# Kernel tuning notes

Hardware: AMD Instinct MI355X
Metric: run time of the kernel (lower is better)

The kernel has to match this reference:

```python
import jax, jax.numpy as jnp
import numpy as np

B, D, S, U, H = 2, 1024, 2048, 1024, 16
LN_EPS = 1e-5

def setup_inputs() -> dict:
    key = jax.random.key(0)
    ks = jax.random.split(key, 5)
    std = 0.02
    return {
        "inputs": jax.random.normal(ks[0], (B, D, S), jnp.float32),
        "Wq": jax.random.normal(ks[1], (D, U), jnp.float32) * std,
        "bq": jnp.zeros((U,), jnp.float32),
        "Wk": jax.random.normal(ks[2], (D, U), jnp.float32) * std,
        "bk": jnp.zeros((U,), jnp.float32),
        "Wv": jax.random.normal(ks[3], (D, U), jnp.float32) * std,
        "bv": jnp.zeros((U,), jnp.float32),
        "Wo": jax.random.normal(ks[4], (U, D), jnp.float32) * std,
        "bo": jnp.zeros((D,), jnp.float32),
        "gamma": jnp.ones((D,), jnp.float32),
        "beta": jnp.zeros((D,), jnp.float32),
        "num_heads": H,
    }

def reference(inputs, Wq, bq, Wk, bk, Wv, bv, Wo, bo, gamma, beta, num_heads):
    # inputs: (B, D, S) -> (B, S, D)
    x = jnp.transpose(inputs, (0, 2, 1))
    b, s, d = x.shape

    def proj(W, bias):
        y = jax.nn.relu(x @ W + bias)               # (b, s, U)
        y = y.reshape(b, s, num_heads, -1)
        return jnp.transpose(y, (0, 2, 1, 3))       # (b, h, s, hd)

    Q = proj(Wq, bq)
    K = proj(Wk, bk)
    V = proj(Wv, bv)
    hd = Q.shape[-1]
    scale = 1.0 / np.sqrt(hd).astype(np.float32)

    # Block-wise flash attention in the source is mathematically plain softmax attention
    # (per-block epsilon 1e-10 is negligible); scale applied to Q, no mask, no dropout.
    scores = jnp.einsum('bhid,bhjd->bhij', Q * scale, K)   # (b, h, s, s)
    P = jax.nn.softmax(scores, axis=-1)
    O = jnp.einsum('bhij,bhjd->bhid', P, V)                # (b, h, s, hd)

    O = jnp.transpose(O, (0, 2, 1, 3)).reshape(b, s, -1)   # (b, s, U)
    out = O @ Wo + bo + x                                  # residual add
    mean = jnp.mean(out, axis=-1, keepdims=True)
    var = jnp.var(out, axis=-1, keepdims=True)
    y = (out - mean) * jax.lax.rsqrt(var + LN_EPS) * gamma + beta
    return jnp.transpose(y, (0, 2, 1))                     # (B, D, S)
```

## Files before the change

### kernel.cpp

```cpp
#include <hip/hip_runtime.h>
#include <hip/hip_bf16.h>

typedef __bf16 bf16x8 __attribute__((ext_vector_type(8)));
typedef __bf16 bf16x4 __attribute__((ext_vector_type(4)));
typedef float  f32x4  __attribute__((ext_vector_type(4)));
typedef float  f32x16 __attribute__((ext_vector_type(16)));

#define MFMA16(a, b, c) __builtin_amdgcn_mfma_f32_16x16x32_bf16((a), (b), (c), 0, 0, 0)
#define MFMA32(a, b, c) __builtin_amdgcn_mfma_f32_32x32x16_bf16((a), (b), (c), 0, 0, 0)

namespace {
constexpr int Bb = 2, Dd = 1024, Ss = 2048, Uu = 1024, Hh = 16;
}

#if __has_builtin(__builtin_amdgcn_exp2f)
#define EXP2(x) __builtin_amdgcn_exp2f(x)
#else
#define EXP2(x) __expf((x) * 0.6931471805599453f)
#endif

__device__ __forceinline__ uint32_t pkbf(float a, float b) {
  union { __bf16 h[2]; uint32_t u; } z;
  z.h[0] = (__bf16)a; z.h[1] = (__bf16)b;
  return z.u;
}
#define PLSWAP(a, b) asm("v_permlane32_swap_b32 %0, %1" : "+v"(a), "+v"(b))

__device__ __forceinline__ void gl16(const void* g, void* l) {
  __builtin_amdgcn_global_load_lds((const __attribute__((address_space(1))) uint32_t*)g,
                                   (__attribute__((address_space(3))) uint32_t*)l, 16, 0, 0);
}

#define VMW(n) asm volatile("s_waitcnt vmcnt(" #n ")" ::: "memory")
#define BARRIER_PIN() do { __builtin_amdgcn_s_barrier(); \
  asm volatile("" ::: "memory"); __builtin_amdgcn_sched_barrier(0); } while (0)
#define LGKM0() asm volatile("s_waitcnt lgkmcnt(0)" ::: "memory")

__global__ __launch_bounds__(256) void k_xpose_x(const float* __restrict__ inp,
                                                 __bf16* __restrict__ xb, float* __restrict__ xt) {
  __shared__ __attribute__((aligned(16))) float xs[64][65];
  const int s0 = blockIdx.x * 64, d0 = blockIdx.y * 64, b = blockIdx.z;
  const int t = threadIdx.x;
  {
    const int i = t >> 2, c = (t & 3) * 16;
    const float* src = inp + ((size_t)(b * Dd + d0 + i)) * Ss + s0 + c;
#pragma unroll
    for (int q = 0; q < 4; ++q) {
      const float4 f = *(const float4*)(src + q * 4);
      xs[i][c + q * 4 + 0] = f.x; xs[i][c + q * 4 + 1] = f.y;
      xs[i][c + q * 4 + 2] = f.z; xs[i][c + q * 4 + 3] = f.w;
    }
  }
  __syncthreads();
  {
    const int sl = t >> 2, dc = (t & 3) * 16;
    float* dstf = xt + ((size_t)(b * Ss + s0 + sl)) * Dd + d0 + dc;
    bf16x8 va, vb;
#pragma unroll
    for (int q = 0; q < 4; ++q) {
      float4 f;
      f.x = xs[dc + q * 4 + 0][sl]; f.y = xs[dc + q * 4 + 1][sl];
      f.z = xs[dc + q * 4 + 2][sl]; f.w = xs[dc + q * 4 + 3][sl];
      *(float4*)(dstf + q * 4) = f;
    }
#pragma unroll
    for (int j = 0; j < 8; ++j) { va[j] = (__bf16)xs[dc + j][sl]; vb[j] = (__bf16)xs[dc + 8 + j][sl]; }
    __bf16* dst = xb + ((size_t)(b * Ss + s0 + sl)) * Dd + d0 + dc;
    *(bf16x8*)dst = va;
    *(bf16x8*)(dst + 8) = vb;
  }
}

__global__ __launch_bounds__(256) void k_xpose_w(const float* __restrict__ w0, const float* __restrict__ w1,
                                                 const float* __restrict__ w2, const float* __restrict__ w3,
                                                 __bf16* __restrict__ o0, __bf16* __restrict__ o1,
                                                 __bf16* __restrict__ o2, __bf16* __restrict__ o3) {
  __shared__ __attribute__((aligned(16))) __bf16 ts[64][72];
  const float* src_m; __bf16* dst_m;
  switch (blockIdx.z) {
    case 0: src_m = w0; dst_m = o0; break;
    case 1: src_m = w1; dst_m = o1; break;
    case 2: src_m = w2; dst_m = o2; break;
    default: src_m = w3; dst_m = o3; break;
  }
  const int n0 = blockIdx.x * 64, k0 = blockIdx.y * 64;
  const int t = threadIdx.x;
  {
    const int i = t >> 2, c = (t & 3) * 16;
    const float* src = src_m + (size_t)(k0 + i) * 1024 + n0 + c;
#pragma unroll
    for (int q = 0; q < 4; ++q) {
      const float4 f = *(const float4*)(src + q * 4);
      ts[i][c + q * 4 + 0] = (__bf16)f.x;
      ts[i][c + q * 4 + 1] = (__bf16)f.y;
      ts[i][c + q * 4 + 2] = (__bf16)f.z;
      ts[i][c + q * 4 + 3] = (__bf16)f.w;
    }
  }
  __syncthreads();
  {
    const int nl = t >> 2, kc = (t & 3) * 16;
    bf16x8 va, vb;
#pragma unroll
    for (int j = 0; j < 8; ++j) { va[j] = ts[kc + j][nl]; vb[j] = ts[kc + 8 + j][nl]; }
    __bf16* dst = dst_m + (size_t)(n0 + nl) * 1024 + k0 + kc;
    *(bf16x8*)dst = va;
    *(bf16x8*)(dst + 8) = vb;
  }
}

__global__ __launch_bounds__(512, 2) void k_gemm_qkv8(const __bf16* __restrict__ A,
    const __bf16* __restrict__ W0, const __bf16* __restrict__ W1, const __bf16* __restrict__ W2,
    const float* __restrict__ b0, const float* __restrict__ b1, const float* __restrict__ b2,
    __bf16* __restrict__ Qb, __bf16* __restrict__ Kb, __bf16* __restrict__ Vt) {
  __shared__ __attribute__((aligned(16))) __bf16 As[4][256][32];
  __shared__ __attribute__((aligned(16))) __bf16 Bs[4][256][32];
  const int t = threadIdx.x;
  const int w = t >> 6, l = t & 63, lg = l >> 4, lr = l & 15;
  const int wm = w >> 2, wn = w & 3;
  const int bid = blockIdx.x;
  const int logical = (bid & 7) * 24 + (bid >> 3);
  const int z = logical >> 6;
  const int rem = logical & 63;
  const int n0 = (rem & 3) * 256, m0 = (rem >> 2) * 256;
  const __bf16* Bt = z == 0 ? W0 : z == 1 ? W1 : W2;
  const float* bias = z == 0 ? b0 : z == 1 ? b1 : b2;

  const int srow = t >> 2, sc8 = t & 3, scol = sc8 * 8;
  const int so = ((sc8 + 4 - ((srow >> 1) & 3)) & 3) * 8;
  const __bf16* gaB = A  + ((size_t)(m0 + srow)) * 1024 + so;
  const __bf16* gbB = Bt + ((size_t)(n0 + srow)) * 1024 + so;
#define STG_A(s, h, kt) gl16(gaB + (size_t)(h) * 128 * 1024 + (kt) * 32, &As[s][(h) * 128 + srow][scol])
#define STG_B(s, h, kt) gl16(gbB + (size_t)(h) * 128 * 1024 + (kt) * 32, &Bs[s][(h) * 128 + srow][scol])

  STG_A(0, 0, 0); STG_A(0, 1, 0); STG_B(0, 0, 0); STG_B(0, 1, 0);
  STG_A(1, 0, 1); STG_A(1, 1, 1); STG_B(1, 0, 1); STG_B(1, 1, 1);
  STG_A(2, 0, 2); STG_A(2, 1, 2); STG_B(2, 0, 2); STG_B(2, 1, 2);
  f32x4 acc[8][4] = {};
  VMW(8);
  BARRIER_PIN();

  const int rdc = ((lg + (lr >> 1)) & 3) * 8;
  const __bf16* Abase = &As[0][0][0] + wm * 4096 + lr * 32 + rdc;
  const __bf16* Bbase = &Bs[0][0][0] + wn * 2048 + lr * 32 + rdc;

  for (int kt = 0; kt < 32; ++kt) {
    const int sC = kt & 3, sS = (kt + 3) & 3;
    const __bf16* Ap = Abase + sC * 8192;
    const __bf16* Bp = Bbase + sC * 8192;
    bf16x8 a0, a1, a2, a3, bb0, bb1, bb2, bb3;
    a0 = *(const bf16x8*)(Ap);         a1 = *(const bf16x8*)(Ap + 512);
    a2 = *(const bf16x8*)(Ap + 1024);  a3 = *(const bf16x8*)(Ap + 1536);
    bb0 = *(const bf16x8*)(Bp);        bb1 = *(const bf16x8*)(Bp + 512);
    bb2 = *(const bf16x8*)(Bp + 1024); bb3 = *(const bf16x8*)(Bp + 1536);
    if (kt < 29) { STG_A(sS, 0, kt + 3); STG_A(sS, 1, kt + 3); }
    BARRIER_PIN();
    LGKM0(); __builtin_amdgcn_sched_barrier(0);
    __builtin_amdgcn_s_setprio(1);
    acc[0][0] = MFMA16(a0, bb0, acc[0][0]); acc[0][1] = MFMA16(a0, bb1, acc[0][1]);
    acc[0][2] = MFMA16(a0, bb2, acc[0][2]); acc[0][3] = MFMA16(a0, bb3, acc[0][3]);
    acc[1][0] = MFMA16(a1, bb0, acc[1][0]); acc[1][1] = MFMA16(a1, bb1, acc[1][1]);
    acc[1][2] = MFMA16(a1, bb2, acc[1][2]); acc[1][3] = MFMA16(a1, bb3, acc[1][3]);
    acc[2][0] = MFMA16(a2, bb0, acc[2][0]); acc[2][1] = MFMA16(a2, bb1, acc[2][1]);
    acc[2][2] = MFMA16(a2, bb2, acc[2][2]); acc[2][3] = MFMA16(a2, bb3, acc[2][3]);
    acc[3][0] = MFMA16(a3, bb0, acc[3][0]); acc[3][1] = MFMA16(a3, bb1, acc[3][1]);
    acc[3][2] = MFMA16(a3, bb2, acc[3][2]); acc[3][3] = MFMA16(a3, bb3, acc[3][3]);
    __builtin_amdgcn_s_setprio(0);
    BARRIER_PIN();
    a0 = *(const bf16x8*)(Ap + 2048);  a1 = *(const bf16x8*)(Ap + 2560);
    a2 = *(const bf16x8*)(Ap + 3072);  a3 = *(const bf16x8*)(Ap + 3584);
    if (kt < 29) { STG_B(sS, 0, kt + 3); STG_B(sS, 1, kt + 3); }
    if (kt < 29) { VMW(8); } else if (kt == 29) { VMW(4); } else if (kt == 30) { VMW(0); }
    BARRIER_PIN();
    LGKM0(); __builtin_amdgcn_sched_barrier(0);
    __builtin_amdgcn_s_setprio(1);
    acc[4][0] = MFMA16(a0, bb0, acc[4][0]); acc[4][1] = MFMA16(a0, bb1, acc[4][1]);
    acc[4][2] = MFMA16(a0, bb2, acc[4][2]); acc[4][3] = MFMA16(a0, bb3, acc[4][3]);
    acc[5][0] = MFMA16(a1, bb0, acc[5][0]); acc[5][1] = MFMA16(a1, bb1, acc[5][1]);
    acc[5][2] = MFMA16(a1, bb2, acc[5][2]); acc[5][3] = MFMA16(a1, bb3, acc[5][3]);
    acc[6][0] = MFMA16(a2, bb0, acc[6][0]); acc[6][1] = MFMA16(a2, bb1, acc[6][1]);
    acc[6][2] = MFMA16(a2, bb2, acc[6][2]); acc[6][3] = MFMA16(a2, bb3, acc[6][3]);
    acc[7][0] = MFMA16(a3, bb0, acc[7][0]); acc[7][1] = MFMA16(a3, bb1, acc[7][1]);
    acc[7][2] = MFMA16(a3, bb2, acc[7][2]); acc[7][3] = MFMA16(a3, bb3, acc[7][3]);
    __builtin_amdgcn_s_setprio(0);
    BARRIER_PIN();
  }
#undef STG_A
#undef STG_B

  const int b = m0 >> 11, sb = m0 & 2047;
  __bf16* Ct = &As[0][0][0];
  float bi[4];
#pragma unroll
  for (int j = 0; j < 4; ++j) bi[j] = bias[n0 + wn * 64 + j * 16 + lr];
  if (z < 2) {
    __bf16* out = z == 0 ? Qb : Kb;
    const float scale = z == 0 ? 0.125f * 1.44269504f : 1.0f;
    const int h0 = n0 >> 6;
    for (int c = 0; c < 4; ++c) {
      __syncthreads();
      if (wm == (c >> 1)) {
        const int q = c & 1;
#pragma unroll
        for (int j = 0; j < 4; ++j) {
          const int nl = wn * 64 + j * 16 + lr;
#pragma unroll
          for (int i2 = 0; i2 < 4; ++i2)
#pragma unroll
            for (int r = 0; r < 4; ++r)
              Ct[(i2 * 16 + lg * 4 + r) * 264 + nl] =
                  (__bf16)(fmaxf(acc[q * 4 + i2][j][r] + bi[j], 0.0f) * scale);
        }
      }
      __syncthreads();
#pragma unroll
      for (int u4 = 0; u4 < 4; ++u4) {
        const int u = u4 * 512 + t;
        const int sl = u >> 5, ru = u & 31;
        const int hh = ru >> 3, sg = ru & 7;
        const bf16x8 v = *(const bf16x8*)&Ct[sl * 264 + hh * 64 + sg * 8];
        *(bf16x8*)(out + ((size_t)(b * Hh + h0 + hh) * Ss + sb + c * 64 + sl) * 64 + sg * 8) = v;
      }
    }
  } else {
    for (int c = 0; c < 4; ++c) {
      __syncthreads();
      if (wn == c) {
#pragma unroll
        for (int j = 0; j < 4; ++j) {
          const int nli = j * 16 + lr;
#pragma unroll
          for (int mi = 0; mi < 8; ++mi)
#pragma unroll
            for (int r2 = 0; r2 < 4; r2 += 2) {
              const int ml = wm * 128 + mi * 16 + lg * 4 + r2;
              const uint32_t pk = pkbf(fmaxf(acc[mi][j][r2] + bi[j], 0.0f),
                                       fmaxf(acc[mi][j][r2 + 1] + bi[j], 0.0f));
              *(uint32_t*)&Ct[nli * 264 + ml] = pk;
            }
        }
      }
      __syncthreads();
#pragma unroll
      for (int u4 = 0; u4 < 4; ++u4) {
        const int u = u4 * 512 + t;
        const int nl = u >> 5, sg = u & 31;
        const bf16x8 v = *(const bf16x8*)&Ct[nl * 264 + sg * 8];
        *(bf16x8*)(Vt + (size_t)(b * 1024 + n0 + c * 64 + nl) * Ss + sb + sg * 8) = v;
      }
    }
  }
}

__device__ __forceinline__ int swz_slot(int row, int slot) { return (slot + (row >> 1)) & 3; }

__device__ __forceinline__ void gemm_core(const __bf16* __restrict__ A, const __bf16* __restrict__ Bt,
                                          __bf16 (*__restrict__ As)[128][32], __bf16 (*__restrict__ Bs)[128][32],
                                          int m0, int n0, int t, f32x4 acc[4][4]) {
  const int w = t >> 6, l = t & 63;
  const int wm = (w >> 1) * 64, wn = (w & 1) * 64;
  const int lg = l >> 4, lr = l & 15;
  const int sr = t >> 2, sc8 = t & 3;
  const int so = ((sc8 + 4 - ((sr >> 1) & 3)) & 3) * 8;
  const __bf16* ga = A + (size_t)(m0 + sr) * 1024 + so;
  const __bf16* gb = Bt + (size_t)(n0 + sr) * 1024 + so;
  const int de = sr * 32 + sc8 * 8;
#define STG(bf, kk) { \
    gl16(ga + (kk) * 32,             &As[bf][0][0] + de); \
    gl16(ga + (kk) * 32 + 64 * 1024, &As[bf][0][0] + de + 64 * 32); \
    gl16(gb + (kk) * 32,             &Bs[bf][0][0] + de); \
    gl16(gb + (kk) * 32 + 64 * 1024, &Bs[bf][0][0] + de + 64 * 32); }
  STG(0, 0) STG(1, 1)
  for (int s = 0; s < 32; ++s) {
    if (s < 31) { VMW(4); } else { VMW(0); }
    BARRIER_PIN();
    if (s + 2 < 32) { const int b2 = (s + 2) % 3; STG(b2, s + 2) }
    const int cb = s % 3;
    bf16x8 af[4], bfr[4];
#pragma unroll
    for (int i = 0; i < 4; ++i) { const int rr = wm + i * 16 + lr; af[i]  = *(const bf16x8*)&As[cb][rr][swz_slot(rr, lg) * 8]; }
#pragma unroll
    for (int i = 0; i < 4; ++i) { const int rr = wn + i * 16 + lr; bfr[i] = *(const bf16x8*)&Bs[cb][rr][swz_slot(rr, lg) * 8]; }
#pragma unroll
    for (int i = 0; i < 4; ++i)
#pragma unroll
      for (int j = 0; j < 4; ++j) acc[i][j] = MFMA16(af[i], bfr[j], acc[i][j]);
  }
#undef STG
}

__global__ __launch_bounds__(256) void k_gemm_o(const __bf16* __restrict__ A, const __bf16* __restrict__ Bt,
                                                const float* __restrict__ bias, const float* __restrict__ xt,
                                                float* __restrict__ Wb, float* __restrict__ partials) {
  __shared__ __attribute__((aligned(16))) char smem[49152];
  auto As = (__bf16 (*)[128][32])smem;
  auto Bs = (__bf16 (*)[128][32])(smem + 24576);
  float* Cs = (float*)smem;
  const int flat = blockIdx.x;
  const int logical = (flat & 7) * 32 + (flat >> 3);
  const int n0 = (logical & 7) * 128, m0 = (logical >> 3) * 128;
  const int t = threadIdx.x, w = t >> 6, l = t & 63;
  const int wm = (w >> 1) * 64, wn = (w & 1) * 64;
  const int lg = l >> 4, lr = l & 15;
  f32x4 acc[4][4] = {};
  gemm_core(A, Bt, As, Bs, m0, n0, t, acc);
  const int sub = t & 31, rid0 = t >> 5;
#pragma unroll
  for (int h2 = 0; h2 < 2; ++h2) {
    __syncthreads();
    if ((w >> 1) == h2) {
#pragma unroll
      for (int j = 0; j < 4; ++j) {
        const int nl = wn + j * 16 + lr;
        const float bi = bias[n0 + nl];
#pragma unroll
        for (int i = 0; i < 4; ++i)
#pragma unroll
          for (int r = 0; r < 4; ++r)
            Cs[(i * 16 + lg * 4 + r) * 132 + nl] = acc[i][j][r] + bi;
      }
    }
    __syncthreads();
#pragma unroll
    for (int p = 0; p < 8; ++p) {
      const int row = p * 8 + rid0;
      const int m = m0 + h2 * 64 + row;
      float4 v = *(const float4*)&Cs[row * 132 + sub * 4];
      const float4 x4 = *(const float4*)&xt[(size_t)m * 1024 + n0 + sub * 4];
      v.x += x4.x; v.y += x4.y; v.z += x4.z; v.w += x4.w;
      *(float4*)&Wb[(size_t)m * 1024 + n0 + sub * 4] = v;
      float s = v.x + v.y + v.z + v.w;
      float q = v.x * v.x + v.y * v.y + v.z * v.z + v.w * v.w;
      s += __shfl_xor(s, 1); s += __shfl_xor(s, 2); s += __shfl_xor(s, 4); s += __shfl_xor(s, 8);
      q += __shfl_xor(q, 1); q += __shfl_xor(q, 2); q += __shfl_xor(q, 4); q += __shfl_xor(q, 8);
      if ((sub & 15) == 0) {
        const int ci = (n0 >> 6) + (sub >> 4);
        partials[((size_t)m * 16 + ci) * 2]     = s;
        partials[((size_t)m * 16 + ci) * 2 + 1] = q;
      }
    }
  }
}

__global__ __launch_bounds__(256, 2) void k_attn6(const __bf16* __restrict__ Qg, const __bf16* __restrict__ Kg,
                                                  const __bf16* __restrict__ Vt, __bf16* __restrict__ Og) {
  __shared__ __attribute__((aligned(16))) char smem[36864];
  auto Ks = (__bf16 (*)[64][72])smem;
  auto Vs = (__bf16 (*)[64][72])(smem + 18432);
  __bf16* Os = (__bf16*)smem;
  const int t = threadIdx.x, l = t & 63, w = t >> 6;
  const int ln = l & 31, hi = l >> 5;
  const int bid = blockIdx.x;
  const int orig = (bid & 7) * 64 + (bid >> 3);
  const int bh = orig >> 4, qt = orig & 15;
  const int q0blk = qt * 128;
  const int q0w = q0blk + w * 32;
  const int b = bh >> 4, h = bh & 15;
  const size_t kbase = (size_t)bh * Ss * 64;
  const int srow = t >> 2, scol = (t & 3) * 16;
  const __bf16* Krow = Kg + kbase + (size_t)srow * 64 + scol;
  const __bf16* Vrow = Vt + (size_t)(bh * 64 + srow) * Ss + scol;

  bf16x8 qf0, qf1, qf2, qf3;
  {
    const __bf16* qp = Qg + kbase + (size_t)(q0w + ln) * 64 + hi * 8;
    qf0 = *(const bf16x8*)(qp);
    qf1 = *(const bf16x8*)(qp + 16);
    qf2 = *(const bf16x8*)(qp + 32);
    qf3 = *(const bf16x8*)(qp + 48);
  }
  f32x16 oA = {}, oB = {};
  float lrow = 0.f;

  auto tile_compute = [&](const __bf16 (&K)[64][72], const __bf16 (&V)[64][72]) {
    f32x16 s0 = {}, s1 = {};
    {
      bf16x8 kf;
#define QK(u, cc, sacc) \
      kf = *(const bf16x8*)&K[(u) * 32 + ln][(cc) * 16 + hi * 8]; \
      sacc = MFMA32(kf, qf##cc, sacc);
      QK(0, 0, s0) QK(0, 1, s0) QK(0, 2, s0) QK(0, 3, s0)
      QK(1, 0, s1) QK(1, 1, s1) QK(1, 2, s1) QK(1, 3, s1)
#undef QK
    }
#pragma unroll
    for (int r = 0; r < 16; ++r) s0[r] = EXP2(s0[r]);
#pragma unroll
    for (int r = 0; r < 16; ++r) s1[r] = EXP2(s1[r]);
    float sm[16];
#pragma unroll
    for (int r = 0; r < 8; ++r) sm[r] = s0[2 * r] + s0[2 * r + 1];
#pragma unroll
    for (int r = 0; r < 8; ++r) sm[8 + r] = s1[2 * r] + s1[2 * r + 1];
#pragma unroll
    for (int st = 8; st > 0; st >>= 1)
#pragma unroll
      for (int r = 0; r < st; ++r) sm[r] += sm[r + st];
    lrow += sm[0];
    uint32_t w0[8], w1[8];
#pragma unroll
    for (int k = 0; k < 8; ++k) w0[k] = pkbf(s0[2 * k], s0[2 * k + 1]);
#pragma unroll
    for (int k = 0; k < 8; ++k) w1[k] = pkbf(s1[2 * k], s1[2 * k + 1]);
    PLSWAP(w0[0], w0[2]); PLSWAP(w0[1], w0[3]);
    PLSWAP(w0[4], w0[6]); PLSWAP(w0[5], w0[7]);
    PLSWAP(w1[0], w1[2]); PLSWAP(w1[1], w1[3]);
    PLSWAP(w1[4], w1[6]); PLSWAP(w1[5], w1[7]);
    union U4 { uint32_t u[4]; bf16x8 v; };
    U4 z;
    bf16x8 pa0, pa1, pa2, pa3;
    z.u[0] = w0[0]; z.u[1] = w0[1]; z.u[2] = w0[2]; z.u[3] = w0[3]; pa0 = z.v;
    z.u[0] = w0[4]; z.u[1] = w0[5]; z.u[2] = w0[6]; z.u[3] = w0[7]; pa1 = z.v;
    z.u[0] = w1[0]; z.u[1] = w1[1]; z.u[2] = w1[2]; z.u[3] = w1[3]; pa2 = z.v;
    z.u[0] = w1[4]; z.u[1] = w1[5]; z.u[2] = w1[6]; z.u[3] = w1[7]; pa3 = z.v;
    {
      bf16x8 vf;
#define PV(half, ti, pa, oacc) \
      vf = *(const bf16x8*)&V[(half) * 32 + ln][(ti) * 16 + hi * 8]; \
      oacc = MFMA32(vf, pa, oacc);
      PV(0, 0, pa0, oA) PV(0, 1, pa1, oA) PV(0, 2, pa2, oA) PV(0, 3, pa3, oA)
      PV(1, 0, pa0, oB) PV(1, 1, pa1, oB) PV(1, 2, pa2, oB) PV(1, 3, pa3, oB)
#undef PV
    }
  };

  bf16x8 kA0 = *(const bf16x8*)(Krow),      kA1 = *(const bf16x8*)(Krow + 8);
  bf16x8 vA0 = *(const bf16x8*)(Vrow),      vA1 = *(const bf16x8*)(Vrow + 8);
  bf16x8 kB0 = *(const bf16x8*)(Krow + 64 * 64), kB1 = *(const bf16x8*)(Krow + 64 * 64 + 8);
  bf16x8 vB0 = *(const bf16x8*)(Vrow + 64), vB1 = *(const bf16x8*)(Vrow + 64 + 8);

  for (int tt = 0; tt < 16; ++tt) {
    *(bf16x8*)&Ks[0][srow][scol]     = kA0;
    *(bf16x8*)&Ks[0][srow][scol + 8] = kA1;
    *(bf16x8*)&Vs[0][srow][scol]     = vA0;
    *(bf16x8*)&Vs[0][srow][scol + 8] = vA1;
    LGKM0();
    BARRIER_PIN();
    if (tt < 15) {
      const size_t ko = (size_t)(2 * tt + 2) * 64;
      kA0 = *(const bf16x8*)(Krow + ko * 64);
      kA1 = *(const bf16x8*)(Krow + ko * 64 + 8);
      vA0 = *(const bf16x8*)(Vrow + ko);
      vA1 = *(const bf16x8*)(Vrow + ko + 8);
    }
    tile_compute(Ks[0], Vs[0]);
    *(bf16x8*)&Ks[1][srow][scol]     = kB0;
    *(bf16x8*)&Ks[1][srow][scol + 8] = kB1;
    *(bf16x8*)&Vs[1][srow][scol]     = vB0;
    *(bf16x8*)&Vs[1][srow][scol + 8] = vB1;
    LGKM0();
    BARRIER_PIN();
    if (tt < 15) {
      const size_t ko = (size_t)(2 * tt + 3) * 64;
      kB0 = *(const bf16x8*)(Krow + ko * 64);
      kB1 = *(const bf16x8*)(Krow + ko * 64 + 8);
      vB0 = *(const bf16x8*)(Vrow + ko);
      vB1 = *(const bf16x8*)(Vrow + ko + 8);
    }
    tile_compute(Ks[1], Vs[1]);
  }
  {
    uint32_t a = __builtin_bit_cast(uint32_t, lrow), bsw = a;
    PLSWAP(a, bsw);
    lrow = __builtin_bit_cast(float, a) + __builtin_bit_cast(float, bsw);
  }
  const float rl = 1.0f / lrow;
  __syncthreads();
  const int ql = w * 32 + ln;
#pragma unroll
  for (int r0 = 0; r0 < 4; ++r0)
#pragma unroll
    for (int j = 0; j < 4; ++j) {
      Os[ql * 68 + hi * 4 + r0 * 8 + j]      = (__bf16)(oA[r0 * 4 + j] * rl);
      Os[ql * 68 + 32 + hi * 4 + r0 * 8 + j] = (__bf16)(oB[r0 * 4 + j] * rl);
    }
  __syncthreads();
  const int sub = t & 7, rid0 = t >> 3;
#pragma unroll
  for (int p = 0; p < 4; ++p) {
    const int rid = p * 32 + rid0;
    const bf16x8 v = *(const bf16x8*)&Os[rid * 68 + sub * 8];
    *(bf16x8*)(Og + ((size_t)(b * Ss + q0blk + rid)) * Uu + h * 64 + sub * 8) = v;
  }
}

__global__ __launch_bounds__(256) void k_ln_stats(const float* __restrict__ partials, float* __restrict__ stats) {
  const int row = blockIdx.x * 256 + threadIdx.x;
  float s = 0.f, q = 0.f;
#pragma unroll
  for (int c = 0; c < 16; ++c) {
    s += partials[((size_t)row * 16 + c) * 2];
    q += partials[((size_t)row * 16 + c) * 2 + 1];
  }
  const float mean = s * (1.0f / 1024.0f);
  const float var = q * (1.0f / 1024.0f) - mean * mean;
  stats[row * 2] = mean;
  stats[row * 2 + 1] = rsqrtf(var + 1e-5f);
}

__global__ __launch_bounds__(256) void k_ln_write(const float* __restrict__ Wb, const float* __restrict__ stats,
                                                  const float* __restrict__ gamma, const float* __restrict__ beta,
                                                  float* __restrict__ out) {
  __shared__ __attribute__((aligned(16))) float ws0[64][65];
  __shared__ float sm[64][2];
  const int d0 = blockIdx.x * 64, s0 = blockIdx.y * 64, b = blockIdx.z;
  const int t = threadIdx.x;
  {
    const int sl = t >> 2, dc = (t & 3) * 16;
    const float* src = Wb + ((size_t)(b * Ss + s0 + sl)) * Dd + d0 + dc;
#pragma unroll
    for (int q = 0; q < 4; ++q) {
      const float4 f = *(const float4*)(src + q * 4);
      ws0[dc + q * 4 + 0][sl] = f.x; ws0[dc + q * 4 + 1][sl] = f.y;
      ws0[dc + q * 4 + 2][sl] = f.z; ws0[dc + q * 4 + 3][sl] = f.w;
    }
  }
  if (t < 128) sm[t >> 1][t & 1] = stats[(size_t)(b * Ss + s0 + (t >> 1)) * 2 + (t & 1)];
  __syncthreads();
  const int dl = t >> 2, sc = (t & 3) * 16;
  const float g = gamma[d0 + dl], be = beta[d0 + dl];
  float* dst = out + ((size_t)(b * Dd + d0 + dl)) * Ss + s0 + sc;
#pragma unroll
  for (int q = 0; q < 4; ++q) {
    float4 o;
    o.x = (ws0[dl][sc + q * 4 + 0] - sm[sc + q * 4 + 0][0]) * sm[sc + q * 4 + 0][1] * g + be;
    o.y = (ws0[dl][sc + q * 4 + 1] - sm[sc + q * 4 + 1][0]) * sm[sc + q * 4 + 1][1] * g + be;
    o.z = (ws0[dl][sc + q * 4 + 2] - sm[sc + q * 4 + 2][0]) * sm[sc + q * 4 + 2][1] * g + be;
    o.w = (ws0[dl][sc + q * 4 + 3] - sm[sc + q * 4 + 3][0]) * sm[sc + q * 4 + 3][1] * g + be;
    *(float4*)(dst + q * 4) = o;
  }
}

extern "C" void kernel_launch(void* const* d_in, const int* in_sizes, int n_in,
                              void* d_out, int out_size, void* d_ws, size_t ws_size,
                              hipStream_t stream) {
  const float* inp   = (const float*)d_in[0];
  const float* Wq    = (const float*)d_in[1];
  const float* bq    = (const float*)d_in[2];
  const float* Wk    = (const float*)d_in[3];
  const float* bk    = (const float*)d_in[4];
  const float* Wv    = (const float*)d_in[5];
  const float* bv    = (const float*)d_in[6];
  const float* Wo    = (const float*)d_in[7];
  const float* bo    = (const float*)d_in[8];
  const float* gamma = (const float*)d_in[9];
  const float* beta  = (const float*)d_in[10];

  char* ws = (char*)d_ws;
  const size_t MB = 1ull << 20;
  __bf16* xb  = (__bf16*)(ws);
  __bf16* Wqt = (__bf16*)(ws + 8 * MB);
  __bf16* Wkt = (__bf16*)(ws + 10 * MB);
  __bf16* Wvt = (__bf16*)(ws + 12 * MB);
  __bf16* Wot = (__bf16*)(ws + 14 * MB);
  __bf16* Qb  = (__bf16*)(ws + 16 * MB);
  __bf16* Kb  = (__bf16*)(ws + 24 * MB);
  __bf16* Vtb = (__bf16*)(ws + 32 * MB);
  __bf16* Ob  = (__bf16*)(ws + 40 * MB);
  float*  xt  = (float*)(ws + 48 * MB);
  float*  Wb  = (float*)(ws + 16 * MB);
  float*  partials = (float*)(ws + 8 * MB);
  float*  stats    = (float*)(ws + 8 * MB + 512 * 1024);

  k_xpose_x<<<dim3(32, 16, 2), 256, 0, stream>>>(inp, xb, xt);
  k_xpose_w<<<dim3(16, 16, 4), 256, 0, stream>>>(Wq, Wk, Wv, Wo, Wqt, Wkt, Wvt, Wot);
  k_gemm_qkv8<<<dim3(192), 512, 0, stream>>>(xb, Wqt, Wkt, Wvt, bq, bk, bv, Qb, Kb, Vtb);
  k_attn6<<<dim3(512), 256, 0, stream>>>(Qb, Kb, Vtb, Ob);
  k_gemm_o<<<dim3(256), 256, 0, stream>>>(Ob, Wot, bo, xt, Wb, partials);
  k_ln_stats<<<dim3(16), 256, 0, stream>>>(partials, stats);
  k_ln_write<<<dim3(16, 32, 2), 256, 0, stream>>>(Wb, stats, gamma, beta, (float*)d_out);
}
```

Before: 141.2 us.

## Use bf16 residual and pre-norm buffers; restructure attention into 128-thread single-buffer blocks

```diff
diff --git a/kernel.cpp b/kernel.cpp
--- a/kernel.cpp
+++ b/kernel.cpp
@@ -37,8 +37,8 @@
 #define LGKM0() asm volatile("s_waitcnt lgkmcnt(0)" ::: "memory")
 
 __global__ __launch_bounds__(256) void k_xpose_x(const float* __restrict__ inp,
-                                                 __bf16* __restrict__ xb, float* __restrict__ xt) {
-  __shared__ __attribute__((aligned(16))) float xs[64][65];
+                                                 __bf16* __restrict__ xb) {
+  __shared__ __attribute__((aligned(16))) __bf16 ts[64][72];
   const int s0 = blockIdx.x * 64, d0 = blockIdx.y * 64, b = blockIdx.z;
   const int t = threadIdx.x;
   {
@@ -47,24 +47,18 @@
 #pragma unroll
     for (int q = 0; q < 4; ++q) {
       const float4 f = *(const float4*)(src + q * 4);
-      xs[i][c + q * 4 + 0] = f.x; xs[i][c + q * 4 + 1] = f.y;
-      xs[i][c + q * 4 + 2] = f.z; xs[i][c + q * 4 + 3] = f.w;
+      ts[i][c + q * 4 + 0] = (__bf16)f.x;
+      ts[i][c + q * 4 + 1] = (__bf16)f.y;
+      ts[i][c + q * 4 + 2] = (__bf16)f.z;
+      ts[i][c + q * 4 + 3] = (__bf16)f.w;
     }
   }
   __syncthreads();
   {
     const int sl = t >> 2, dc = (t & 3) * 16;
-    float* dstf = xt + ((size_t)(b * Ss + s0 + sl)) * Dd + d0 + dc;
     bf16x8 va, vb;
 #pragma unroll
-    for (int q = 0; q < 4; ++q) {
-      float4 f;
-      f.x = xs[dc + q * 4 + 0][sl]; f.y = xs[dc + q * 4 + 1][sl];
-      f.z = xs[dc + q * 4 + 2][sl]; f.w = xs[dc + q * 4 + 3][sl];
-      *(float4*)(dstf + q * 4) = f;
-    }
-#pragma unroll
-    for (int j = 0; j < 8; ++j) { va[j] = (__bf16)xs[dc + j][sl]; vb[j] = (__bf16)xs[dc + 8 + j][sl]; }
+    for (int j = 0; j < 8; ++j) { va[j] = ts[dc + j][sl]; vb[j] = ts[dc + 8 + j][sl]; }
     __bf16* dst = xb + ((size_t)(b * Ss + s0 + sl)) * Dd + d0 + dc;
     *(bf16x8*)dst = va;
     *(bf16x8*)(dst + 8) = vb;
@@ -290,8 +284,8 @@
 }
 
 __global__ __launch_bounds__(256) void k_gemm_o(const __bf16* __restrict__ A, const __bf16* __restrict__ Bt,
-                                                const float* __restrict__ bias, const float* __restrict__ xt,
-                                                float* __restrict__ Wb, float* __restrict__ partials) {
+                                                const float* __restrict__ bias, const __bf16* __restrict__ xb,
+                                                __bf16* __restrict__ Wb, float* __restrict__ partials) {
   __shared__ __attribute__((aligned(16))) char smem[49152];
   auto As = (__bf16 (*)[128][32])smem;
   auto Bs = (__bf16 (*)[128][32])(smem + 24576);
@@ -326,9 +320,11 @@
       const int row = p * 8 + rid0;
       const int m = m0 + h2 * 64 + row;
       float4 v = *(const float4*)&Cs[row * 132 + sub * 4];
-      const float4 x4 = *(const float4*)&xt[(size_t)m * 1024 + n0 + sub * 4];
-      v.x += x4.x; v.y += x4.y; v.z += x4.z; v.w += x4.w;
-      *(float4*)&Wb[(size_t)m * 1024 + n0 + sub * 4] = v;
+      const bf16x4 x4 = *(const bf16x4*)&xb[(size_t)m * 1024 + n0 + sub * 4];
+      v.x += (float)x4[0]; v.y += (float)x4[1]; v.z += (float)x4[2]; v.w += (float)x4[3];
+      bf16x4 pv;
+      pv[0] = (__bf16)v.x; pv[1] = (__bf16)v.y; pv[2] = (__bf16)v.z; pv[3] = (__bf16)v.w;
+      *(bf16x4*)&Wb[(size_t)m * 1024 + n0 + sub * 4] = pv;
       float s = v.x + v.y + v.z + v.w;
       float q = v.x * v.x + v.y * v.y + v.z * v.z + v.w * v.w;
       s += __shfl_xor(s, 1); s += __shfl_xor(s, 2); s += __shfl_xor(s, 4); s += __shfl_xor(s, 8);
@@ -342,24 +338,22 @@
   }
 }
 
-__global__ __launch_bounds__(256, 2) void k_attn6(const __bf16* __restrict__ Qg, const __bf16* __restrict__ Kg,
+__global__ __launch_bounds__(128, 2) void k_attn7(const __bf16* __restrict__ Qg, const __bf16* __restrict__ Kg,
                                                   const __bf16* __restrict__ Vt, __bf16* __restrict__ Og) {
-  __shared__ __attribute__((aligned(16))) char smem[36864];
-  auto Ks = (__bf16 (*)[64][72])smem;
-  auto Vs = (__bf16 (*)[64][72])(smem + 18432);
-  __bf16* Os = (__bf16*)smem;
+  __shared__ __attribute__((aligned(16))) __bf16 Ks[64][72];
+  __shared__ __attribute__((aligned(16))) __bf16 Vs[64][72];
   const int t = threadIdx.x, l = t & 63, w = t >> 6;
   const int ln = l & 31, hi = l >> 5;
   const int bid = blockIdx.x;
-  const int orig = (bid & 7) * 64 + (bid >> 3);
-  const int bh = orig >> 4, qt = orig & 15;
-  const int q0blk = qt * 128;
+  const int orig = (bid & 7) * 128 + (bid >> 3);
+  const int bh = orig >> 5, qt = orig & 31;
+  const int q0blk = qt * 64;
   const int q0w = q0blk + w * 32;
   const int b = bh >> 4, h = bh & 15;
   const size_t kbase = (size_t)bh * Ss * 64;
-  const int srow = t >> 2, scol = (t & 3) * 16;
-  const __bf16* Krow = Kg + kbase + (size_t)srow * 64 + scol;
-  const __bf16* Vrow = Vt + (size_t)(bh * 64 + srow) * Ss + scol;
+  const int srow = t >> 1, sc2 = (t & 1) * 32;
+  const __bf16* Kro = Kg + kbase + (size_t)srow * 64 + sc2;
+  const __bf16* Vro = Vt + ((size_t)(bh * 64 + srow)) * Ss + sc2;
 
   bf16x8 qf0, qf1, qf2, qf3;
   {
@@ -372,12 +366,12 @@
   f32x16 oA = {}, oB = {};
   float lrow = 0.f;
 
-  auto tile_compute = [&](const __bf16 (&K)[64][72], const __bf16 (&V)[64][72]) {
+  auto tile_compute = [&]() {
     f32x16 s0 = {}, s1 = {};
     {
       bf16x8 kf;
 #define QK(u, cc, sacc) \
-      kf = *(const bf16x8*)&K[(u) * 32 + ln][(cc) * 16 + hi * 8]; \
+      kf = *(const bf16x8*)&Ks[(u) * 32 + ln][(cc) * 16 + hi * 8]; \
       sacc = MFMA32(kf, qf##cc, sacc);
       QK(0, 0, s0) QK(0, 1, s0) QK(0, 2, s0) QK(0, 3, s0)
       QK(1, 0, s1) QK(1, 1, s1) QK(1, 2, s1) QK(1, 3, s1)
@@ -416,7 +410,7 @@
     {
       bf16x8 vf;
 #define PV(half, ti, pa, oacc) \
-      vf = *(const bf16x8*)&V[(half) * 32 + ln][(ti) * 16 + hi * 8]; \
+      vf = *(const bf16x8*)&Vs[(half) * 32 + ln][(ti) * 16 + hi * 8]; \
       oacc = MFMA32(vf, pa, oacc);
       PV(0, 0, pa0, oA) PV(0, 1, pa1, oA) PV(0, 2, pa2, oA) PV(0, 3, pa3, oA)
       PV(1, 0, pa0, oB) PV(1, 1, pa1, oB) PV(1, 2, pa2, oB) PV(1, 3, pa3, oB)
@@ -424,40 +418,30 @@
     }
   };
 
-  bf16x8 kA0 = *(const bf16x8*)(Krow),      kA1 = *(const bf16x8*)(Krow + 8);
-  bf16x8 vA0 = *(const bf16x8*)(Vrow),      vA1 = *(const bf16x8*)(Vrow + 8);
-  bf16x8 kB0 = *(const bf16x8*)(Krow + 64 * 64), kB1 = *(const bf16x8*)(Krow + 64 * 64 + 8);
-  bf16x8 vB0 = *(const bf16x8*)(Vrow + 64), vB1 = *(const bf16x8*)(Vrow + 64 + 8);
-
-  for (int tt = 0; tt < 16; ++tt) {
-    *(bf16x8*)&Ks[0][srow][scol]     = kA0;
-    *(bf16x8*)&Ks[0][srow][scol + 8] = kA1;
-    *(bf16x8*)&Vs[0][srow][scol]     = vA0;
-    *(bf16x8*)&Vs[0][srow][scol + 8] = vA1;
+  bf16x8 kst[4], vst[4];
+#pragma unroll
+  for (int u = 0; u < 4; ++u) {
+    kst[u] = *(const bf16x8*)(Kro + u * 8);
+    vst[u] = *(const bf16x8*)(Vro + u * 8);
+  }
+  for (int tt = 0; tt < 32; ++tt) {
+#pragma unroll
+    for (int u = 0; u < 4; ++u) {
+      *(bf16x8*)&Ks[srow][sc2 + u * 8] = kst[u];
+      *(bf16x8*)&Vs[srow][sc2 + u * 8] = vst[u];
+    }
     LGKM0();
     BARRIER_PIN();
-    if (tt < 15) {
-      const size_t ko = (size_t)(2 * tt + 2) * 64;
-      kA0 = *(const bf16x8*)(Krow + ko * 64);
-      kA1 = *(const bf16x8*)(Krow + ko * 64 + 8);
-      vA0 = *(const bf16x8*)(Vrow + ko);
-      vA1 = *(const bf16x8*)(Vrow + ko + 8);
-    }
-    tile_compute(Ks[0], Vs[0]);
-    *(bf16x8*)&Ks[1][srow][scol]     = kB0;
-    *(bf16x8*)&Ks[1][srow][scol + 8] = kB1;
-    *(bf16x8*)&Vs[1][srow][scol]     = vB0;
-    *(bf16x8*)&Vs[1][srow][scol + 8] = vB1;
-    LGKM0();
-    BARRIER_PIN();
-    if (tt < 15) {
-      const size_t ko = (size_t)(2 * tt + 3) * 64;
-      kB0 = *(const bf16x8*)(Krow + ko * 64);
-      kB1 = *(const bf16x8*)(Krow + ko * 64 + 8);
-      vB0 = *(const bf16x8*)(Vrow + ko);
-      vB1 = *(const bf16x8*)(Vrow + ko + 8);
-    }
-    tile_compute(Ks[1], Vs[1]);
+    if (tt < 31) {
+      const size_t ko = (size_t)(tt + 1) * 64;
+#pragma unroll
+      for (int u = 0; u < 4; ++u) {
+        kst[u] = *(const bf16x8*)(Kro + ko * 64 + u * 8);
+        vst[u] = *(const bf16x8*)(Vro + ko + u * 8);
+      }
+    }
+    tile_compute();
+    BARRIER_PIN();
   }
   {
     uint32_t a = __builtin_bit_cast(uint32_t, lrow), bsw = a;
@@ -465,7 +449,7 @@
     lrow = __builtin_bit_cast(float, a) + __builtin_bit_cast(float, bsw);
   }
   const float rl = 1.0f / lrow;
-  __syncthreads();
+  __bf16* Os = &Ks[0][0];
   const int ql = w * 32 + ln;
 #pragma unroll
   for (int r0 = 0; r0 < 4; ++r0)
@@ -478,7 +462,7 @@
   const int sub = t & 7, rid0 = t >> 3;
 #pragma unroll
   for (int p = 0; p < 4; ++p) {
-    const int rid = p * 32 + rid0;
+    const int rid = p * 16 + rid0;
     const bf16x8 v = *(const bf16x8*)&Os[rid * 68 + sub * 8];
     *(bf16x8*)(Og + ((size_t)(b * Ss + q0blk + rid)) * Uu + h * 64 + sub * 8) = v;
   }
@@ -498,7 +482,7 @@
   stats[row * 2 + 1] = rsqrtf(var + 1e-5f);
 }
 
-__global__ __launch_bounds__(256) void k_ln_write(const float* __restrict__ Wb, const float* __restrict__ stats,
+__global__ __launch_bounds__(256) void k_ln_write(const __bf16* __restrict__ Wb, const float* __restrict__ stats,
                                                   const float* __restrict__ gamma, const float* __restrict__ beta,
                                                   float* __restrict__ out) {
   __shared__ __attribute__((aligned(16))) float ws0[64][65];
@@ -507,13 +491,11 @@
   const int t = threadIdx.x;
   {
     const int sl = t >> 2, dc = (t & 3) * 16;
-    const float* src = Wb + ((size_t)(b * Ss + s0 + sl)) * Dd + d0 + dc;
-#pragma unroll
-    for (int q = 0; q < 4; ++q) {
-      const float4 f = *(const float4*)(src + q * 4);
-      ws0[dc + q * 4 + 0][sl] = f.x; ws0[dc + q * 4 + 1][sl] = f.y;
-      ws0[dc + q * 4 + 2][sl] = f.z; ws0[dc + q * 4 + 3][sl] = f.w;
-    }
+    const __bf16* src = Wb + ((size_t)(b * Ss + s0 + sl)) * Dd + d0 + dc;
+    const bf16x8 f0 = *(const bf16x8*)src;
+    const bf16x8 f1 = *(const bf16x8*)(src + 8);
+#pragma unroll
+    for (int j = 0; j < 8; ++j) { ws0[dc + j][sl] = (float)f0[j]; ws0[dc + 8 + j][sl] = (float)f1[j]; }
   }
   if (t < 128) sm[t >> 1][t & 1] = stats[(size_t)(b * Ss + s0 + (t >> 1)) * 2 + (t & 1)];
   __syncthreads();
@@ -557,16 +539,15 @@
   __bf16* Kb  = (__bf16*)(ws + 24 * MB);
   __bf16* Vtb = (__bf16*)(ws + 32 * MB);
   __bf16* Ob  = (__bf16*)(ws + 40 * MB);
-  float*  xt  = (float*)(ws + 48 * MB);
-  float*  Wb  = (float*)(ws + 16 * MB);
+  __bf16* Wb  = (__bf16*)(ws + 16 * MB);
   float*  partials = (float*)(ws + 8 * MB);
   float*  stats    = (float*)(ws + 8 * MB + 512 * 1024);
 
-  k_xpose_x<<<dim3(32, 16, 2), 256, 0, stream>>>(inp, xb, xt);
+  k_xpose_x<<<dim3(32, 16, 2), 256, 0, stream>>>(inp, xb);
   k_xpose_w<<<dim3(16, 16, 4), 256, 0, stream>>>(Wq, Wk, Wv, Wo, Wqt, Wkt, Wvt, Wot);
   k_gemm_qkv8<<<dim3(192), 512, 0, stream>>>(xb, Wqt, Wkt, Wvt, bq, bk, bv, Qb, Kb, Vtb);
-  k_attn6<<<dim3(512), 256, 0, stream>>>(Qb, Kb, Vtb, Ob);
-  k_gemm_o<<<dim3(256), 256, 0, stream>>>(Ob, Wot, bo, xt, Wb, partials);
+  k_attn7<<<dim3(1024), 128, 0, stream>>>(Qb, Kb, Vtb, Ob);
+  k_gemm_o<<<dim3(256), 256, 0, stream>>>(Ob, Wot, bo, xb, Wb, partials);
   k_ln_stats<<<dim3(16), 256, 0, stream>>>(partials, stats);
   k_ln_write<<<dim3(16, 32, 2), 256, 0, stream>>>(Wb, stats, gamma, beta, (float*)d_out);
 }
```

Result: no change. 140.6 us (-0.4%).
